# Performance work log

Measured on AMD Instinct MI355X. Metric: run time of the kernel, lower is better.

Reference implementation:

```python
import jax, jax.numpy as jnp
import numpy as np

N = 50000   # nodes
E = 800000  # edges (avg degree 16)
H = 128     # hidden


def setup_inputs() -> dict:
    key = jax.random.key(0)
    k1, k2, k3, k4, k5 = jax.random.split(key, 5)
    s = 1.0 / np.sqrt(H).astype(np.float32)
    x = jax.random.normal(k1, (N, H), dtype=jnp.float32)
    edge_index = jax.random.randint(k2, (2, E), 0, N, dtype=jnp.int64)
    a_i = jax.random.normal(k3, (H,), dtype=jnp.float32) * s
    a_j = jax.random.normal(k4, (H,), dtype=jnp.float32) * s
    W = jax.random.normal(k5, (H, H), dtype=jnp.float32) * s
    return {"x": x, "edge_index": edge_index, "a_i": a_i, "a_j": a_j, "W": W}


def reference(x, edge_index, a_i, a_j, W):
    n = x.shape[0]
    idx_j = edge_index[0]  # row of sparse adj (output node)
    idx_i = edge_index[1]  # col of sparse adj (source node, softmax segment)

    # per-node attention scores, gathered per edge
    si = x @ a_i  # [N]
    sj = x @ a_j  # [N]
    e = jax.nn.leaky_relu(si[idx_i] + sj[idx_j], negative_slope=0.01)  # [E]

    # segment softmax over idx_i (numerically stable)
    seg_max = jax.ops.segment_max(e, idx_i, num_segments=n)
    e_exp = jnp.exp(e - seg_max[idx_i])
    denom = jax.ops.segment_sum(e_exp, idx_i, num_segments=n)
    alpha = e_exp / denom[idx_i]  # [E]

    # messages and sparse aggregation: out[j] += alpha * m[i]
    m = x + x @ W  # [N, H]
    out = jax.ops.segment_sum(alpha[:, None] * m[idx_i], idx_j, num_segments=n)

    # exact (erf) GELU to match torch nn.GELU default; dropout is identity in eval
    return jax.nn.gelu(out, approximate=False)
```

## Files before the change

### kernel.cpp

```cpp
#include <hip/hip_runtime.h>
#include <hip/hip_fp16.h>
#include <math.h>

#define HDIM 128
#define NB   32
#define CAP  768
#define BINB 256
#define DG   64
#define WIN  12544

typedef __attribute__((ext_vector_type(8))) short short8;
typedef __attribute__((ext_vector_type(4))) float f32x4;

__device__ __forceinline__ float gelu_f(float v) {
    return 0.5f * v * (1.0f + erff(v * 0.70710678118654752440f));
}
__device__ __forceinline__ unsigned bf_rne(float f) {
    unsigned u = __float_as_uint(f);
    return (u + 0x7fffu + ((u >> 16) & 1u)) >> 16;
}
__device__ __forceinline__ float bf_lo(unsigned u) {
    return __uint_as_float(u << 16);
}
__device__ __forceinline__ float bf_hi(unsigned u) {
    return __uint_as_float(u & 0xffff0000u);
}

__global__ void __launch_bounds__(256) k_scores(
    const float* __restrict__ x, const float* __restrict__ a_i,
    const float* __restrict__ a_j, float* __restrict__ si,
    float* __restrict__ sj, unsigned* __restrict__ xbp, int N) {
    const int wave = threadIdx.x >> 6;
    const int lane = threadIdx.x & 63;
    const int n = blockIdx.x * 4 + wave;
    if (n >= N) return;
    const float xa = x[(size_t)n * HDIM + lane];
    const float xb = x[(size_t)n * HDIM + 64 + lane];
    xbp[(size_t)n * 64 + lane] = bf_rne(xa) | (bf_rne(xb) << 16);
    float vi = xa * a_i[lane] + xb * a_i[64 + lane];
    float vj = xa * a_j[lane] + xb * a_j[64 + lane];
    #pragma unroll
    for (int d = 32; d; d >>= 1) {
        vi += __shfl_xor(vi, d, 64);
        vj += __shfl_xor(vj, d, 64);
    }
    if (lane == 0) {
        si[n] = vi;
        sj[n] = vj;
    }
}

__global__ void __launch_bounds__(1024) k_binA(
    const int* __restrict__ idx_i, const int* __restrict__ idx_j,
    const float* __restrict__ si, const float* __restrict__ sj,
    unsigned short* __restrict__ exbuf, unsigned* __restrict__ cnt_g,
    int nbuk, int E_) {
    __shared__ unsigned cnt_l[2048];
    const int blk = blockIdx.x;
    const int chunk = (E_ + BINB - 1) / BINB;
    const int e0 = blk * chunk;
    const int e1 = min(e0 + chunk, E_);
    for (int w = threadIdx.x; w < nbuk; w += 1024) cnt_l[w] = 0u;
    __syncthreads();
    for (int t = e0 + threadIdx.x; t < e1; t += 1024) {
        const int i = idx_i[t];
        const int j = idx_j[t];
        float e = si[i] + sj[j];
        e = (e > 0.f) ? e : 0.01f * e;
        const float ex = __expf(e);
        exbuf[t] = __half_as_ushort(__float2half(ex));
        atomicAdd(&cnt_l[j >> 5], 1u);
    }
    __syncthreads();
    for (int w = threadIdx.x; w < nbuk; w += 1024)
        cnt_g[(size_t)blk * nbuk + w] = cnt_l[w];
}

__global__ void __launch_bounds__(256) k_scan(
    const unsigned* __restrict__ cnt_g, unsigned* __restrict__ base_t,
    unsigned* __restrict__ gcnt, int nbuk) {
    const int bucket = blockIdx.x;
    const int t = threadIdx.x;
    const int lane = t & 63;
    const int wave = t >> 6;
    const unsigned v = cnt_g[(size_t)t * nbuk + bucket];
    unsigned s = v;
    #pragma unroll
    for (int d = 1; d < 64; d <<= 1) {
        const unsigned o = __shfl_up(s, d, 64);
        if (lane >= d) s += o;
    }
    __shared__ unsigned wsum[4];
    if (lane == 63) wsum[wave] = s;
    __syncthreads();
    unsigned add = 0;
    #pragma unroll
    for (int w = 0; w < 4; ++w)
        if (w < wave) add += wsum[w];
    base_t[(size_t)t * nbuk + bucket] = add + s - v;
    if (t == 255) gcnt[bucket] = add + s;
}

__global__ void __launch_bounds__(1024) k_binB(
    const int* __restrict__ idx_i, const int* __restrict__ idx_j,
    const unsigned short* __restrict__ exbuf,
    const unsigned* __restrict__ base_t, uint2* __restrict__ edges,
    int nbuk, int E_) {
    __shared__ unsigned cur[2048];
    const int blk = blockIdx.x;
    const int chunk = (E_ + BINB - 1) / BINB;
    const int e0 = blk * chunk;
    const int e1 = min(e0 + chunk, E_);
    for (int w = threadIdx.x; w < nbuk; w += 1024)
        cur[w] = base_t[(size_t)blk * nbuk + w];
    __syncthreads();
    for (int t = e0 + threadIdx.x; t < e1; t += 1024) {
        const int i = idx_i[t];
        const int j = idx_j[t];
        const float ex = __half2float(__ushort_as_half(exbuf[t]));
        const int b = j >> 5;
        const unsigned slot = min(atomicAdd(&cur[b], 1u), (unsigned)(CAP - 1));
        edges[(size_t)b * CAP + slot] = make_uint2(
            (unsigned)i | ((unsigned)(j & 31) << 24), __float_as_uint(ex));
    }
}

__global__ void __launch_bounds__(1024) k_den(
    const int* __restrict__ idx_i, const unsigned short* __restrict__ exbuf,
    float* __restrict__ denp, int N, int E_) {
    __shared__ float dl[WIN];
    const int cid = blockIdx.x & (DG - 1);
    const int lo = (blockIdx.x >> 6) * WIN;
    const int chunk = (E_ + DG - 1) / DG;
    const int e0 = cid * chunk;
    const int e1 = min(e0 + chunk, E_);
    for (int w = threadIdx.x; w < WIN; w += 1024) dl[w] = 0.f;
    __syncthreads();
    for (int t = e0 + threadIdx.x; t < e1; t += 1024) {
        const unsigned rel = (unsigned)(idx_i[t] - lo);
        if (rel < (unsigned)WIN)
            atomicAdd(&dl[rel], __half2float(__ushort_as_half(exbuf[t])));
    }
    __syncthreads();
    for (int w = threadIdx.x; w < WIN && lo + w < N; w += 1024)
        denp[(size_t)cid * N + lo + w] = dl[w];
}

__global__ void __launch_bounds__(256) k_denred(const float* __restrict__ denp,
                                                float* __restrict__ denom,
                                                int N) {
    const int v = blockIdx.x * 256 + threadIdx.x;
    if (v >= N) return;
    float s = 0.f;
    for (int b = 0; b < DG; ++b) s += denp[(size_t)b * N + v];
    denom[v] = s;
}

__global__ void __launch_bounds__(256) k_gemm(
    const unsigned* __restrict__ xbp, const float* __restrict__ Wm,
    const float* __restrict__ denom, unsigned* __restrict__ mbp, int N) {
    __shared__ unsigned wl[128][68];
    const int t = threadIdx.x;
    {
        const int n = t & 127;
        const int h = t >> 7;
        for (int w = h * 32; w < h * 32 + 32; ++w) {
            const float f0 = Wm[w * 128 + n];
            const float f1 = Wm[(w + 64) * 128 + n];
            wl[n][w] = bf_rne(f0) | (bf_rne(f1) << 16);
        }
    }
    __syncthreads();
    const int wave = t >> 6;
    const int lane = t & 63;
    const int q = lane >> 4;
    const int m16 = lane & 15;
    const int r0 = blockIdx.x * 64 + wave * 16;
    if (r0 >= N) return;
    const int rowA = min(r0 + m16, N - 1);
    union { uint4 u; short8 s; } a[4];
    #pragma unroll
    for (int kb = 0; kb < 4; ++kb)
        a[kb].u = *(const uint4*)(xbp + (size_t)rowA * 64 + kb * 16 + q * 4);
    f32x4 acc[8];
    #pragma unroll
    for (int c = 0; c < 8; ++c) acc[c] = (f32x4){0.f, 0.f, 0.f, 0.f};
    #pragma unroll
    for (int kb = 0; kb < 4; ++kb) {
        #pragma unroll
        for (int c = 0; c < 8; ++c) {
            const short8 bfr =
                *(const short8*)&wl[c * 16 + m16][kb * 16 + q * 4];
            acc[c] = __builtin_amdgcn_mfma_f32_16x16x32_bf16(
                a[kb].s, bfr, acc[c], 0, 0, 0);
        }
    }
    #pragma unroll
    for (int r = 0; r < 4; ++r) {
        const int row = r0 + q * 4 + r;
        if (row >= N) continue;
        const float rdv = 1.0f / denom[row];
        #pragma unroll
        for (int c = 0; c < 4; ++c) {
            const int w = m16 + 16 * c;
            const unsigned xv = xbp[(size_t)row * 64 + w];
            const float vlo = (bf_lo(xv) + acc[c][r]) * rdv;
            const float vhi = (bf_hi(xv) + acc[c + 4][r]) * rdv;
            mbp[(size_t)row * 64 + w] = bf_rne(vlo) | (bf_rne(vhi) << 16);
        }
    }
}

__global__ void __launch_bounds__(512) k_agg(
    const unsigned* __restrict__ gcnt, const uint2* __restrict__ edges,
    const unsigned* __restrict__ mbp, float* __restrict__ out, int N) {
    __shared__ uint2 srec[CAP];
    __shared__ unsigned cnt_l[NB];
    __shared__ unsigned off_l[NB];
    const int b = blockIdx.x;
    const int cntb = min((int)gcnt[b], CAP);
    const uint2* eb = edges + (size_t)b * CAP;
    if (threadIdx.x < NB) cnt_l[threadIdx.x] = 0u;
    __syncthreads();
    uint2 r0_ = make_uint2(0u, 0u), r1_ = make_uint2(0u, 0u);
    int jl0 = -1, jl1 = -1, kl0 = 0, kl1 = 0;
    {
        const int t0 = threadIdx.x;
        if (t0 < cntb) {
            r0_ = eb[t0];
            jl0 = (int)(r0_.x >> 24);
            kl0 = (int)atomicAdd(&cnt_l[jl0], 1u);
        }
        const int t1 = threadIdx.x + 512;
        if (t1 < cntb) {
            r1_ = eb[t1];
            jl1 = (int)(r1_.x >> 24);
            kl1 = (int)atomicAdd(&cnt_l[jl1], 1u);
        }
    }
    __syncthreads();
    if (threadIdx.x < NB) {
        const unsigned v = cnt_l[threadIdx.x];
        unsigned s = v;
        #pragma unroll
        for (int d = 1; d < NB; d <<= 1) {
            const unsigned o = __shfl_up(s, d, 64);
            if ((int)threadIdx.x >= d) s += o;
        }
        off_l[threadIdx.x] = s - v;
    }
    __syncthreads();
    if (jl0 >= 0) srec[off_l[jl0] + kl0] = r0_;
    if (jl1 >= 0) srec[off_l[jl1] + kl1] = r1_;
    __syncthreads();
    const int wave = threadIdx.x >> 6;
    const int lane = threadIdx.x & 63;
    for (int nr = wave; nr < NB; nr += 8) {
        const int n = (b << 5) + nr;
        if (n >= N) continue;
        const int p0 = (int)off_l[nr];
        const int p1 = p0 + (int)cnt_l[nr];
        float ax = 0.f, ay = 0.f;
        int p = p0;
        for (; p + 8 <= p1; p += 8) {
            const uint2 e0 = srec[p];
            const uint2 e1 = srec[p + 1];
            const uint2 e2 = srec[p + 2];
            const uint2 e3 = srec[p + 3];
            const uint2 e4 = srec[p + 4];
            const uint2 e5 = srec[p + 5];
            const uint2 e6 = srec[p + 6];
            const uint2 e7 = srec[p + 7];
            const unsigned u0 = mbp[(size_t)(e0.x & 0xffffffu) * 64 + lane];
            const unsigned u1 = mbp[(size_t)(e1.x & 0xffffffu) * 64 + lane];
            const unsigned u2 = mbp[(size_t)(e2.x & 0xffffffu) * 64 + lane];
            const unsigned u3 = mbp[(size_t)(e3.x & 0xffffffu) * 64 + lane];
            const unsigned u4 = mbp[(size_t)(e4.x & 0xffffffu) * 64 + lane];
            const unsigned u5 = mbp[(size_t)(e5.x & 0xffffffu) * 64 + lane];
            const unsigned u6 = mbp[(size_t)(e6.x & 0xffffffu) * 64 + lane];
            const unsigned u7 = mbp[(size_t)(e7.x & 0xffffffu) * 64 + lane];
            ax = fmaf(__uint_as_float(e0.y), bf_lo(u0), ax);
            ay = fmaf(__uint_as_float(e0.y), bf_hi(u0), ay);
            ax = fmaf(__uint_as_float(e1.y), bf_lo(u1), ax);
            ay = fmaf(__uint_as_float(e1.y), bf_hi(u1), ay);
            ax = fmaf(__uint_as_float(e2.y), bf_lo(u2), ax);
            ay = fmaf(__uint_as_float(e2.y), bf_hi(u2), ay);
            ax = fmaf(__uint_as_float(e3.y), bf_lo(u3), ax);
            ay = fmaf(__uint_as_float(e3.y), bf_hi(u3), ay);
            ax = fmaf(__uint_as_float(e4.y), bf_lo(u4), ax);
            ay = fmaf(__uint_as_float(e4.y), bf_hi(u4), ay);
            ax = fmaf(__uint_as_float(e5.y), bf_lo(u5), ax);
            ay = fmaf(__uint_as_float(e5.y), bf_hi(u5), ay);
            ax = fmaf(__uint_as_float(e6.y), bf_lo(u6), ax);
            ay = fmaf(__uint_as_float(e6.y), bf_hi(u6), ay);
            ax = fmaf(__uint_as_float(e7.y), bf_lo(u7), ax);
            ay = fmaf(__uint_as_float(e7.y), bf_hi(u7), ay);
        }
        for (; p + 4 <= p1; p += 4) {
            const uint2 e0 = srec[p];
            const uint2 e1 = srec[p + 1];
            const uint2 e2 = srec[p + 2];
            const uint2 e3 = srec[p + 3];
            const unsigned u0 = mbp[(size_t)(e0.x & 0xffffffu) * 64 + lane];
            const unsigned u1 = mbp[(size_t)(e1.x & 0xffffffu) * 64 + lane];
            const unsigned u2 = mbp[(size_t)(e2.x & 0xffffffu) * 64 + lane];
            const unsigned u3 = mbp[(size_t)(e3.x & 0xffffffu) * 64 + lane];
            ax = fmaf(__uint_as_float(e0.y), bf_lo(u0), ax);
            ay = fmaf(__uint_as_float(e0.y), bf_hi(u0), ay);
            ax = fmaf(__uint_as_float(e1.y), bf_lo(u1), ax);
            ay = fmaf(__uint_as_float(e1.y), bf_hi(u1), ay);
            ax = fmaf(__uint_as_float(e2.y), bf_lo(u2), ax);
            ay = fmaf(__uint_as_float(e2.y), bf_hi(u2), ay);
            ax = fmaf(__uint_as_float(e3.y), bf_lo(u3), ax);
            ay = fmaf(__uint_as_float(e3.y), bf_hi(u3), ay);
        }
        for (; p < p1; ++p) {
            const uint2 e = srec[p];
            const unsigned u = mbp[(size_t)(e.x & 0xffffffu) * 64 + lane];
            const float a = __uint_as_float(e.y);
            ax = fmaf(a, bf_lo(u), ax);
            ay = fmaf(a, bf_hi(u), ay);
        }
        out[(size_t)n * HDIM + lane] = gelu_f(ax);
        out[(size_t)n * HDIM + 64 + lane] = gelu_f(ay);
    }
}

extern "C" void kernel_launch(void* const* d_in, const int* in_sizes, int n_in,
                              void* d_out, int out_size, void* d_ws,
                              size_t ws_size, hipStream_t stream) {
    const float* x   = (const float*)d_in[0];
    const int*   eix = (const int*)d_in[1];
    const float* a_i = (const float*)d_in[2];
    const float* a_j = (const float*)d_in[3];
    const float* Wm  = (const float*)d_in[4];
    float* out = (float*)d_out;

    const int N = in_sizes[0] / HDIM;
    const int E = in_sizes[1] / 2;
    const int nbuk = (N + NB - 1) / NB;

    unsigned* xbp   = (unsigned*)d_ws;
    unsigned* mbp   = xbp + (size_t)N * 64;
    float* denp     = (float*)(mbp + (size_t)N * 64);
    float* si       = denp + (size_t)DG * N;
    float* sj       = si + N;
    float* denom    = sj + N;
    unsigned* cnt_g = (unsigned*)(denom + N);
    unsigned* base_t = cnt_g + (size_t)BINB * nbuk;
    unsigned* gcnt  = base_t + (size_t)BINB * nbuk;
    unsigned short* exbuf =
        (unsigned short*)(gcnt + ((nbuk + 7) & ~7));
    uint2* edges    = (uint2*)(exbuf + ((E + 7) & ~7));

    const int* idx_j = eix;
    const int* idx_i = eix + E;

    k_scores<<<(N + 3) / 4, 256, 0, stream>>>(x, a_i, a_j, si, sj, xbp, N);
    k_binA<<<BINB, 1024, 0, stream>>>(idx_i, idx_j, si, sj, exbuf, cnt_g,
                                      nbuk, E);
    k_scan<<<nbuk, 256, 0, stream>>>(cnt_g, base_t, gcnt, nbuk);
    k_binB<<<BINB, 1024, 0, stream>>>(idx_i, idx_j, exbuf, base_t, edges,
                                      nbuk, E);
    k_den<<<DG * 4, 1024, 0, stream>>>(idx_i, exbuf, denp, N, E);
    k_denred<<<(N + 255) / 256, 256, 0, stream>>>(denp, denom, N);
    k_gemm<<<(N + 63) / 64, 256, 0, stream>>>(xbp, Wm, denom, mbp, N);
    k_agg<<<nbuk, 512, 0, stream>>>(gcnt, edges, mbp, out, N);
}
```

Before: 169.6 us.

## Aggregate x before applying W, fold softmax normalization into edge weights

Uses linearity to reorder the computation: instead of building m = x + xW per node and gathering m, the aggregation gathers bf16 x directly into a sum s, then applies s + sW with MFMA and fuses GELU into that GEMM epilogue. The per-edge alpha = ex/denom[i] is now computed in the binning pass, which is moved after the denominator reduction. This drops the separate m write/read round trip, but adds a bf16 intermediate (s) written and re-read, plus an extra bf16 rounding on the aggregated sum before the matmul.

```diff
diff --git a/kernel.cpp b/kernel.cpp
--- a/kernel.cpp
+++ b/kernel.cpp
@@ -101,30 +101,6 @@
     if (t == 255) gcnt[bucket] = add + s;
 }
 
-__global__ void __launch_bounds__(1024) k_binB(
-    const int* __restrict__ idx_i, const int* __restrict__ idx_j,
-    const unsigned short* __restrict__ exbuf,
-    const unsigned* __restrict__ base_t, uint2* __restrict__ edges,
-    int nbuk, int E_) {
-    __shared__ unsigned cur[2048];
-    const int blk = blockIdx.x;
-    const int chunk = (E_ + BINB - 1) / BINB;
-    const int e0 = blk * chunk;
-    const int e1 = min(e0 + chunk, E_);
-    for (int w = threadIdx.x; w < nbuk; w += 1024)
-        cur[w] = base_t[(size_t)blk * nbuk + w];
-    __syncthreads();
-    for (int t = e0 + threadIdx.x; t < e1; t += 1024) {
-        const int i = idx_i[t];
-        const int j = idx_j[t];
-        const float ex = __half2float(__ushort_as_half(exbuf[t]));
-        const int b = j >> 5;
-        const unsigned slot = min(atomicAdd(&cur[b], 1u), (unsigned)(CAP - 1));
-        edges[(size_t)b * CAP + slot] = make_uint2(
-            (unsigned)i | ((unsigned)(j & 31) << 24), __float_as_uint(ex));
-    }
-}
-
 __global__ void __launch_bounds__(1024) k_den(
     const int* __restrict__ idx_i, const unsigned short* __restrict__ exbuf,
     float* __restrict__ denp, int N, int E_) {
@@ -156,64 +132,34 @@
     denom[v] = s;
 }
 
-__global__ void __launch_bounds__(256) k_gemm(
-    const unsigned* __restrict__ xbp, const float* __restrict__ Wm,
-    const float* __restrict__ denom, unsigned* __restrict__ mbp, int N) {
-    __shared__ unsigned wl[128][68];
-    const int t = threadIdx.x;
-    {
-        const int n = t & 127;
-        const int h = t >> 7;
-        for (int w = h * 32; w < h * 32 + 32; ++w) {
-            const float f0 = Wm[w * 128 + n];
-            const float f1 = Wm[(w + 64) * 128 + n];
-            wl[n][w] = bf_rne(f0) | (bf_rne(f1) << 16);
-        }
-    }
-    __syncthreads();
-    const int wave = t >> 6;
-    const int lane = t & 63;
-    const int q = lane >> 4;
-    const int m16 = lane & 15;
-    const int r0 = blockIdx.x * 64 + wave * 16;
-    if (r0 >= N) return;
-    const int rowA = min(r0 + m16, N - 1);
-    union { uint4 u; short8 s; } a[4];
-    #pragma unroll
-    for (int kb = 0; kb < 4; ++kb)
-        a[kb].u = *(const uint4*)(xbp + (size_t)rowA * 64 + kb * 16 + q * 4);
-    f32x4 acc[8];
-    #pragma unroll
-    for (int c = 0; c < 8; ++c) acc[c] = (f32x4){0.f, 0.f, 0.f, 0.f};
-    #pragma unroll
-    for (int kb = 0; kb < 4; ++kb) {
-        #pragma unroll
-        for (int c = 0; c < 8; ++c) {
-            const short8 bfr =
-                *(const short8*)&wl[c * 16 + m16][kb * 16 + q * 4];
-            acc[c] = __builtin_amdgcn_mfma_f32_16x16x32_bf16(
-                a[kb].s, bfr, acc[c], 0, 0, 0);
-        }
-    }
-    #pragma unroll
-    for (int r = 0; r < 4; ++r) {
-        const int row = r0 + q * 4 + r;
-        if (row >= N) continue;
-        const float rdv = 1.0f / denom[row];
-        #pragma unroll
-        for (int c = 0; c < 4; ++c) {
-            const int w = m16 + 16 * c;
-            const unsigned xv = xbp[(size_t)row * 64 + w];
-            const float vlo = (bf_lo(xv) + acc[c][r]) * rdv;
-            const float vhi = (bf_hi(xv) + acc[c + 4][r]) * rdv;
-            mbp[(size_t)row * 64 + w] = bf_rne(vlo) | (bf_rne(vhi) << 16);
-        }
+__global__ void __launch_bounds__(1024) k_binB(
+    const int* __restrict__ idx_i, const int* __restrict__ idx_j,
+    const unsigned short* __restrict__ exbuf,
+    const float* __restrict__ denom, const unsigned* __restrict__ base_t,
+    uint2* __restrict__ edges, int nbuk, int E_) {
+    __shared__ unsigned cur[2048];
+    const int blk = blockIdx.x;
+    const int chunk = (E_ + BINB - 1) / BINB;
+    const int e0 = blk * chunk;
+    const int e1 = min(e0 + chunk, E_);
+    for (int w = threadIdx.x; w < nbuk; w += 1024)
+        cur[w] = base_t[(size_t)blk * nbuk + w];
+    __syncthreads();
+    for (int t = e0 + threadIdx.x; t < e1; t += 1024) {
+        const int i = idx_i[t];
+        const int j = idx_j[t];
+        const float ex = __half2float(__ushort_as_half(exbuf[t]));
+        const float alpha = ex / denom[i];
+        const int b = j >> 5;
+        const unsigned slot = min(atomicAdd(&cur[b], 1u), (unsigned)(CAP - 1));
+        edges[(size_t)b * CAP + slot] = make_uint2(
+            (unsigned)i | ((unsigned)(j & 31) << 24), __float_as_uint(alpha));
     }
 }
 
 __global__ void __launch_bounds__(512) k_agg(
     const unsigned* __restrict__ gcnt, const uint2* __restrict__ edges,
-    const unsigned* __restrict__ mbp, float* __restrict__ out, int N) {
+    const unsigned* __restrict__ xbp, unsigned* __restrict__ sbp, int N) {
     __shared__ uint2 srec[CAP];
     __shared__ unsigned cnt_l[NB];
     __shared__ unsigned off_l[NB];
@@ -271,14 +217,14 @@
             const uint2 e5 = srec[p + 5];
             const uint2 e6 = srec[p + 6];
             const uint2 e7 = srec[p + 7];
-            const unsigned u0 = mbp[(size_t)(e0.x & 0xffffffu) * 64 + lane];
-            const unsigned u1 = mbp[(size_t)(e1.x & 0xffffffu) * 64 + lane];
-            const unsigned u2 = mbp[(size_t)(e2.x & 0xffffffu) * 64 + lane];
-            const unsigned u3 = mbp[(size_t)(e3.x & 0xffffffu) * 64 + lane];
-            const unsigned u4 = mbp[(size_t)(e4.x & 0xffffffu) * 64 + lane];
-            const unsigned u5 = mbp[(size_t)(e5.x & 0xffffffu) * 64 + lane];
-            const unsigned u6 = mbp[(size_t)(e6.x & 0xffffffu) * 64 + lane];
-            const unsigned u7 = mbp[(size_t)(e7.x & 0xffffffu) * 64 + lane];
+            const unsigned u0 = xbp[(size_t)(e0.x & 0xffffffu) * 64 + lane];
+            const unsigned u1 = xbp[(size_t)(e1.x & 0xffffffu) * 64 + lane];
+            const unsigned u2 = xbp[(size_t)(e2.x & 0xffffffu) * 64 + lane];
+            const unsigned u3 = xbp[(size_t)(e3.x & 0xffffffu) * 64 + lane];
+            const unsigned u4 = xbp[(size_t)(e4.x & 0xffffffu) * 64 + lane];
+            const unsigned u5 = xbp[(size_t)(e5.x & 0xffffffu) * 64 + lane];
+            const unsigned u6 = xbp[(size_t)(e6.x & 0xffffffu) * 64 + lane];
+            const unsigned u7 = xbp[(size_t)(e7.x & 0xffffffu) * 64 + lane];
             ax = fmaf(__uint_as_float(e0.y), bf_lo(u0), ax);
             ay = fmaf(__uint_as_float(e0.y), bf_hi(u0), ay);
             ax = fmaf(__uint_as_float(e1.y), bf_lo(u1), ax);
@@ -301,10 +247,10 @@
             const uint2 e1 = srec[p + 1];
             const uint2 e2 = srec[p + 2];
             const uint2 e3 = srec[p + 3];
-            const unsigned u0 = mbp[(size_t)(e0.x & 0xffffffu) * 64 + lane];
-            const unsigned u1 = mbp[(size_t)(e1.x & 0xffffffu) * 64 + lane];
-            const unsigned u2 = mbp[(size_t)(e2.x & 0xffffffu) * 64 + lane];
-            const unsigned u3 = mbp[(size_t)(e3.x & 0xffffffu) * 64 + lane];
+            const unsigned u0 = xbp[(size_t)(e0.x & 0xffffffu) * 64 + lane];
+            const unsigned u1 = xbp[(size_t)(e1.x & 0xffffffu) * 64 + lane];
+            const unsigned u2 = xbp[(size_t)(e2.x & 0xffffffu) * 64 + lane];
+            const unsigned u3 = xbp[(size_t)(e3.x & 0xffffffu) * 64 + lane];
             ax = fmaf(__uint_as_float(e0.y), bf_lo(u0), ax);
             ay = fmaf(__uint_as_float(e0.y), bf_hi(u0), ay);
             ax = fmaf(__uint_as_float(e1.y), bf_lo(u1), ax);
@@ -316,13 +262,67 @@
         }
         for (; p < p1; ++p) {
             const uint2 e = srec[p];
-            const unsigned u = mbp[(size_t)(e.x & 0xffffffu) * 64 + lane];
+            const unsigned u = xbp[(size_t)(e.x & 0xffffffu) * 64 + lane];
             const float a = __uint_as_float(e.y);
             ax = fmaf(a, bf_lo(u), ax);
             ay = fmaf(a, bf_hi(u), ay);
         }
-        out[(size_t)n * HDIM + lane] = gelu_f(ax);
-        out[(size_t)n * HDIM + 64 + lane] = gelu_f(ay);
+        sbp[(size_t)n * 64 + lane] = bf_rne(ax) | (bf_rne(ay) << 16);
+    }
+}
+
+__global__ void __launch_bounds__(256) k_out(
+    const unsigned* __restrict__ sbp, const float* __restrict__ Wm,
+    float* __restrict__ out, int N) {
+    __shared__ unsigned wl[128][68];
+    const int t = threadIdx.x;
+    {
+        const int n = t & 127;
+        const int h = t >> 7;
+        for (int w = h * 32; w < h * 32 + 32; ++w) {
+            const float f0 = Wm[w * 128 + n];
+            const float f1 = Wm[(w + 64) * 128 + n];
+            wl[n][w] = bf_rne(f0) | (bf_rne(f1) << 16);
+        }
+    }
+    __syncthreads();
+    const int wave = t >> 6;
+    const int lane = t & 63;
+    const int q = lane >> 4;
+    const int m16 = lane & 15;
+    const int r0 = blockIdx.x * 64 + wave * 16;
+    if (r0 >= N) return;
+    const int rowA = min(r0 + m16, N - 1);
+    union { uint4 u; short8 s; } a[4];
+    #pragma unroll
+    for (int kb = 0; kb < 4; ++kb)
+        a[kb].u = *(const uint4*)(sbp + (size_t)rowA * 64 + kb * 16 + q * 4);
+    f32x4 acc[8];
+    #pragma unroll
+    for (int c = 0; c < 8; ++c) acc[c] = (f32x4){0.f, 0.f, 0.f, 0.f};
+    #pragma unroll
+    for (int kb = 0; kb < 4; ++kb) {
+        #pragma unroll
+        for (int c = 0; c < 8; ++c) {
+            const short8 bfr =
+                *(const short8*)&wl[c * 16 + m16][kb * 16 + q * 4];
+            acc[c] = __builtin_amdgcn_mfma_f32_16x16x32_bf16(
+                a[kb].s, bfr, acc[c], 0, 0, 0);
+        }
+    }
+    #pragma unroll
+    for (int r = 0; r < 4; ++r) {
+        const int row = r0 + q * 4 + r;
+        if (row >= N) continue;
+        #pragma unroll
+        for (int c = 0; c < 4; ++c) {
+            const int w = m16 + 16 * c;
+            const unsigned sv = sbp[(size_t)row * 64 + w];
+            const float vlo = bf_lo(sv) + acc[c][r];
+            const float vhi = bf_hi(sv) + acc[c + 4][r];
+            out[(size_t)row * HDIM + w] = gelu_f(vlo);
+            out[(size_t)row * HDIM + w + 64] = gelu_f(vhi);
+        }
     }
 }
 
@@ -341,8 +341,8 @@
     const int nbuk = (N + NB - 1) / NB;
 
     unsigned* xbp   = (unsigned*)d_ws;
-    unsigned* mbp   = xbp + (size_t)N * 64;
-    float* denp     = (float*)(mbp + (size_t)N * 64);
+    unsigned* sbp   = xbp + (size_t)N * 64;
+    float* denp     = (float*)(sbp + (size_t)N * 64);
     float* si       = denp + (size_t)DG * N;
     float* sj       = si + N;
     float* denom    = sj + N;
@@ -360,10 +360,10 @@
     k_binA<<<BINB, 1024, 0, stream>>>(idx_i, idx_j, si, sj, exbuf, cnt_g,
                                       nbuk, E);
     k_scan<<<nbuk, 256, 0, stream>>>(cnt_g, base_t, gcnt, nbuk);
-    k_binB<<<BINB, 1024, 0, stream>>>(idx_i, idx_j, exbuf, base_t, edges,
-                                      nbuk, E);
     k_den<<<DG * 4, 1024, 0, stream>>>(idx_i, exbuf, denp, N, E);
     k_denred<<<(N + 255) / 256, 256, 0, stream>>>(denp, denom, N);
-    k_gemm<<<(N + 63) / 64, 256, 0, stream>>>(xbp, Wm, denom, mbp, N);
-    k_agg<<<nbuk, 512, 0, stream>>>(gcnt, edges, mbp, out, N);
-}
+    k_binB<<<BINB, 1024, 0, stream>>>(idx_i, idx_j, exbuf, denom, base_t,
+                                      edges, nbuk, E);
+    k_agg<<<nbuk, 512, 0, stream>>>(gcnt, edges, xbp, sbp, N);
+    k_out<<<(N + 63) / 64, 256, 0, stream>>>(sbp, Wm, out, N);
+}
```

New measurement: 174.0 us. 1.03x slower.
